# Kernel tuning notes

Hardware: AMD Instinct MI355X
Metric: run time of the kernel (lower is better)

Reference implementation:

```python
import jax, jax.numpy as jnp
import numpy as np

S, M, E, K, D = 16384, 512, 16, 2, 256
H1, H2, H3 = 500, 500, 1000


def setup_inputs() -> dict:
    key = jax.random.key(0)
    ks = jax.random.split(key, 8)
    p = lambda k, sh: jax.random.normal(k, sh, dtype=jnp.float32) * 0.02
    return {
        "x": jax.random.normal(ks[0], (S, M), dtype=jnp.float32),
        "noise": jax.random.uniform(ks[1], (S, E), dtype=jnp.float32),  # Router's torch.rand noise
        "Wr": p(ks[2], (E, M)),                       # router weight (Linear, no bias)
        "W1": p(ks[3], (E, M, H1)), "b1": jnp.zeros((E, H1), jnp.float32),
        "W2": p(ks[4], (E, H1, H2)), "b2": jnp.zeros((E, H2), jnp.float32),
        "W3": p(ks[5], (E, H2, H3)), "b3": jnp.zeros((E, H3), jnp.float32),
        "W4": p(ks[6], (E, H3, D)), "b4": jnp.zeros((E, D), jnp.float32),
    }


def reference(x, noise, Wr, W1, b1, W2, b2, W3, b3, W4, b4):
    # Router: zero-init linear + uniform noise
    logits = x @ Wr.T + noise                      # [S,E]
    select = jax.nn.softmax(logits, axis=1)        # [S,E]
    gate, index = jax.lax.top_k(select, K)         # [S,K]
    gate = gate / gate.sum(axis=1, keepdims=True)
    mask = jax.nn.one_hot(index, E, dtype=jnp.float32)  # [S,K,E]

    # load-balance loss
    density = mask.sum(axis=1).mean(axis=0)        # [E]
    density_proxy = select.mean(axis=0)            # [E]
    balance_loss = (density_proxy * density).mean() * float(E ** 2)

    # combine tensor: mask_flat is all-ones, so combine = sum_k gate_k * one_hot_k
    final_weight = (gate[:, :, None] * mask).sum(axis=1)     # [S,E]
    dispatch = (final_weight > 0).astype(x.dtype)            # bool->float, [S,E]
    select0 = dispatch

    # dense one-hot dispatch: expert_inputs[e,s,:] = x[s,:] * dispatch[s,e]
    expert_inputs = jnp.einsum('sm,se->esm', x, dispatch)    # [E,S,M]

    # per-expert Encoder MLP, vectorized over experts
    h = jax.nn.relu(jnp.einsum('esm,emh->esh', expert_inputs, W1) + b1[:, None, :])
    h = jax.nn.relu(jnp.einsum('esh,ehg->esg', h, W2) + b2[:, None, :])
    h = jax.nn.relu(jnp.einsum('esg,egf->esf', h, W3) + b3[:, None, :])
    expert_out = jnp.einsum('esf,efd->esd', h, W4) + b4[:, None, :]  # [E,S,D]

    final_output = jnp.einsum('se,esd->sd', final_weight, expert_out)  # [S,D]
    dist_loss = jnp.float32(0.0)  # t=False path
    return final_output, select0, balance_loss, dist_loss
```

## Files before the change

kernel.cpp:

```cpp
#include <hip/hip_runtime.h>
#include <stdint.h>

#define S_TOK 16384
#define M_DIM 512
#define E_EXP 16
#define D_OUT 256
#define H1D 500
#define H2D 500
#define H3D 1000

typedef float f32x4 __attribute__((ext_vector_type(4)));
typedef long lx2 __attribute__((ext_vector_type(2)));
typedef int i32x2 __attribute__((ext_vector_type(2)));

template <bool HI>
__device__ __forceinline__ int pk8(float a, float b, int old) {
  return __builtin_amdgcn_cvt_pk_fp8_f32(a, b, old, HI);
}
__device__ __forceinline__ unsigned char f2fp8(float f) {
  return (unsigned char)(__builtin_amdgcn_cvt_pk_fp8_f32(f, 0.f, 0, false) & 0xff);
}

__device__ __forceinline__ void ld_lds16(const unsigned char* g, unsigned char* l) {
  __builtin_amdgcn_global_load_lds(
      (const __attribute__((address_space(1))) unsigned int*)(const void*)g,
      (__attribute__((address_space(3))) unsigned int*)(void*)l, 16, 0, 0);
}

struct TokenRec { int i1, i2; float g1, g2; };

__global__ __launch_bounds__(256) void k_router(const float* __restrict__ x,
                                                const float* __restrict__ noise,
                                                const float* __restrict__ Wr,
                                                float* __restrict__ sel_out,
                                                float* __restrict__ sel_buf,
                                                TokenRec* __restrict__ te) {
  __shared__ float wr[E_EXP * 516];
  int t = threadIdx.x;
  for (int i = t; i < E_EXP * M_DIM; i += 256) {
    int e = i >> 9, m = i & 511;
    wr[e * 516 + m] = Wr[i];
  }
  __syncthreads();

  int wv = t >> 6, l = t & 63;
  int e = l & 15, tg = l >> 4;
  int s = blockIdx.x * 16 + wv * 4 + tg;

  const float* xr = x + (size_t)s * M_DIM;
  const float* wre = &wr[e * 516];
  double a0 = 0.0, a1 = 0.0, a2 = 0.0, a3 = 0.0;
#pragma unroll 4
  for (int m = 0; m < M_DIM; m += 4) {
    f32x4 xv = *(const f32x4*)(xr + m);
    f32x4 wv4 = *(const f32x4*)(wre + m);
    a0 += (double)xv.x * (double)wv4.x;
    a1 += (double)xv.y * (double)wv4.y;
    a2 += (double)xv.z * (double)wv4.z;
    a3 += (double)xv.w * (double)wv4.w;
  }
  double a = (a0 + a1) + (a2 + a3);
  a += (double)noise[(size_t)s * E_EXP + e];

  double mx = a;
#pragma unroll
  for (int off = 8; off >= 1; off >>= 1) { double o = __shfl_xor(mx, off, 64); mx = (o > mx) ? o : mx; }
  double p = exp(a - mx);
  double sum = p;
#pragma unroll
  for (int off = 8; off >= 1; off >>= 1) sum += __shfl_xor(sum, off, 64);
  sel_buf[(size_t)s * E_EXP + e] = (float)(p / sum);

  unsigned long long pb = __double_as_longlong(p);
  unsigned long long key = (pb & ~0xFFull) | (unsigned long long)(255 - e);
  unsigned long long k1 = key;
#pragma unroll
  for (int off = 8; off >= 1; off >>= 1) { unsigned long long o = __shfl_xor(k1, off, 64); k1 = (o > k1) ? o : k1; }
  int i1 = 255 - (int)(k1 & 0xFFull);
  unsigned long long key2 = (e == i1) ? 0ull : key;
  unsigned long long k2 = key2;
#pragma unroll
  for (int off = 8; off >= 1; off >>= 1) { unsigned long long o = __shfl_xor(k2, off, 64); k2 = (o > k2) ? o : k2; }
  int i2 = 255 - (int)(k2 & 0xFFull);

  double p1 = __shfl(p, tg * 16 + i1, 64);
  double p2 = __shfl(p, tg * 16 + i2, 64);

  sel_out[(size_t)s * E_EXP + e] = (e == i1 || e == i2) ? 1.f : 0.f;
  if (e == 0) {
    double inv = 1.0 / (p1 + p2);
    TokenRec r; r.i1 = i1; r.i2 = i2; r.g1 = (float)(p1 * inv); r.g2 = (float)(p2 * inv);
    te[s] = r;
  }
}

__global__ __launch_bounds__(256) void k_stats(const float* __restrict__ sel_buf,
                                               const TokenRec* __restrict__ te,
                                               float* __restrict__ partials) {
  __shared__ float psum[256];
  __shared__ unsigned int hist[E_EXP];
  int t = threadIdx.x, b = blockIdx.x;
  if (t < E_EXP) hist[t] = 0u;
  __syncthreads();
  int e = t & 15, rg = t >> 4;
  int base = b * 1024;
  float acc = 0.f;
#pragma unroll 4
  for (int i = 0; i < 64; i++)
    acc += sel_buf[(size_t)(base + i * 16 + rg) * E_EXP + e];
  for (int i = t; i < 1024; i += 256) {
    TokenRec r = te[base + i];
    atomicAdd(&hist[r.i1], 1u);
    atomicAdd(&hist[r.i2], 1u);
  }
  psum[t] = acc;
  __syncthreads();
  if (t < E_EXP) {
    float v = 0.f;
#pragma unroll
    for (int rg2 = 0; rg2 < 16; rg2++) v += psum[rg2 * 16 + t];
    partials[b * 32 + t] = v;
    partials[b * 32 + 16 + t] = (float)hist[t];
  }
}

__global__ void k_prefix_loss(const float* __restrict__ partials,
                              unsigned int* __restrict__ counts,
                              unsigned int* __restrict__ offsets,
                              unsigned int* __restrict__ cursor,
                              float* __restrict__ out_loss) {
  __shared__ float pr[E_EXP];
  __shared__ unsigned int cn[E_EXP];
  int t = threadIdx.x;
  if (t < E_EXP) {
    float p = 0.f, c = 0.f;
    for (int b = 0; b < 16; b++) { p += partials[b * 32 + t]; c += partials[b * 32 + 16 + t]; }
    pr[t] = p; cn[t] = (unsigned int)(c + 0.5f);
    cursor[t] = 0u;
  }
  __syncthreads();
  if (t == 0) {
    unsigned int acc = 0; float ls = 0.f;
    for (int e = 0; e < E_EXP; e++) {
      counts[e] = cn[e];
      offsets[e] = acc;
      acc += cn[e];
      ls += pr[e] * (float)cn[e];
    }
    out_loss[0] = ls * ((float)E_EXP / ((float)S_TOK * (float)S_TOK));
    out_loss[1] = 0.f;
  }
}

__global__ __launch_bounds__(256) void k_listbuild(const TokenRec* __restrict__ te,
                                                   const unsigned int* __restrict__ offsets,
                                                   unsigned int* __restrict__ cursor,
                                                   int* __restrict__ slot_token,
                                                   float* __restrict__ slot_gate,
                                                   int* __restrict__ tok_slot) {
  __shared__ unsigned int lhist[E_EXP];
  __shared__ unsigned int lbase[E_EXP];
  __shared__ unsigned int lcur[E_EXP];
  int t = threadIdx.x, b = blockIdx.x;
  int base = b * 1024;
  if (t < E_EXP) lhist[t] = 0u;
  __syncthreads();
  for (int i = t; i < 1024; i += 256) {
    TokenRec r = te[base + i];
    atomicAdd(&lhist[r.i1], 1u);
    atomicAdd(&lhist[r.i2], 1u);
  }
  __syncthreads();
  if (t < E_EXP) {
    lbase[t] = offsets[t] + atomicAdd(&cursor[t], lhist[t]);
    lcur[t] = 0u;
  }
  __syncthreads();
  for (int i = t; i < 1024; i += 256) {
    int s = base + i;
    TokenRec r = te[s];
    unsigned int p1 = atomicAdd(&lcur[r.i1], 1u);
    int sl1 = (int)(lbase[r.i1] + p1);
    slot_token[sl1] = s; slot_gate[sl1] = r.g1;
    unsigned int p2 = atomicAdd(&lcur[r.i2], 1u);
    int sl2 = (int)(lbase[r.i2] + p2);
    slot_token[sl2] = s; slot_gate[sl2] = r.g2;
    tok_slot[2 * s] = sl1;
    tok_slot[2 * s + 1] = sl2;
  }
}

__global__ __launch_bounds__(256) void k_gather(const float* __restrict__ x,
                                                const int* __restrict__ slot_token,
                                                unsigned char* __restrict__ xg) {
  int idx = blockIdx.x * 256 + threadIdx.x;
  int row = idx >> 6, t6 = idx & 63;
  int blk = t6 >> 3, q = (t6 >> 1) & 3, h = t6 & 1;
  int tkn = slot_token[row];
  const float* xp = x + (size_t)tkn * M_DIM + blk * 64 + h * 32 + q * 8;
  f32x4 v0 = *(const f32x4*)xp;
  f32x4 v1 = *(const f32x4*)(xp + 4);
  int b0 = pk8<false>(v0.x, v0.y, 0); b0 = pk8<true>(v0.z, v0.w, b0);
  int b1 = pk8<false>(v1.x, v1.y, 0); b1 = pk8<true>(v1.z, v1.w, b1);
  i32x2 o; o.x = b0; o.y = b1;
  *(i32x2*)&xg[(size_t)row * 512 + blk * 64 + q * 16 + h * 8] = o;
}

__global__ __launch_bounds__(256) void k_convw_all(const float* __restrict__ W1,
                                                   const float* __restrict__ W2,
                                                   const float* __restrict__ W3,
                                                   const float* __restrict__ W4,
                                                   unsigned char* __restrict__ D1,
                                                   unsigned char* __restrict__ D2,
                                                   unsigned char* __restrict__ D3,
                                                   unsigned char* __restrict__ D4) {
  __shared__ float tile[64][65];
  int tb = blockIdx.x, e = blockIdx.y;
  const float* src; unsigned char* dst;
  int Kr, Nr, Kp, Np, kx, ny;
  if (tb < 64)        { src = W1; dst = D1; Kr = 512;  Nr = H1D; Kp = 512;  Np = 512;  kx = tb >> 3;  ny = tb & 7; }
  else if (tb < 128)  { tb -= 64;  src = W2; dst = D2; Kr = H1D; Nr = H2D; Kp = 512;  Np = 512;  kx = tb >> 3;  ny = tb & 7; }
  else if (tb < 256)  { tb -= 128; src = W3; dst = D3; Kr = H2D; Nr = H3D; Kp = 512;  Np = 1024; kx = tb >> 4;  ny = tb & 15; }
  else                { tb -= 256; src = W4; dst = D4; Kr = H3D; Nr = 256; Kp = 1024; Np = 256;  kx = tb >> 2;  ny = tb & 3; }
  int k0 = kx * 64, n0 = ny * 64;
  int t = threadIdx.x;
  int cx = t & 63, ry = t >> 6;
  const float* sp = src + (size_t)e * Kr * Nr;
#pragma unroll
  for (int i = 0; i < 16; i++) {
    int k = k0 + ry + i * 4, n = n0 + cx;
    float v = (k < Kr && n < Nr) ? sp[(size_t)k * Nr + n] : 0.f;
    tile[ry + i * 4][cx] = v;
  }
  __syncthreads();
  int nl = t >> 2, q = t & 3;
  int b0 = pk8<false>(tile[q * 8 + 0][nl], tile[q * 8 + 1][nl], 0);
  b0 = pk8<true>(tile[q * 8 + 2][nl], tile[q * 8 + 3][nl], b0);
  int b1 = pk8<false>(tile[q * 8 + 4][nl], tile[q * 8 + 5][nl], 0);
  b1 = pk8<true>(tile[q * 8 + 6][nl], tile[q * 8 + 7][nl], b1);
  int c0 = pk8<false>(tile[32 + q * 8 + 0][nl], tile[32 + q * 8 + 1][nl], 0);
  c0 = pk8<true>(tile[32 + q * 8 + 2][nl], tile[32 + q * 8 + 3][nl], c0);
  int c1 = pk8<false>(tile[32 + q * 8 + 4][nl], tile[32 + q * 8 + 5][nl], 0);
  c1 = pk8<true>(tile[32 + q * 8 + 6][nl], tile[32 + q * 8 + 7][nl], c1);
  uint4 pk; pk.x = (unsigned)b0; pk.y = (unsigned)b1; pk.z = (unsigned)c0; pk.w = (unsigned)c1;
  *(uint4*)&dst[(size_t)e * Np * Kp + (size_t)(n0 + nl) * Kp + k0 + q * 16] = pk;
}

__global__ __launch_bounds__(256, 4) void k_gemm_mid(const unsigned char* __restrict__ in,
                                                  const unsigned char* __restrict__ wt,
                                                  const float* __restrict__ bias,
                                                  unsigned char* __restrict__ out,
                                                  const unsigned int* __restrict__ offsets,
                                                  const unsigned int* __restrict__ counts,
                                                  int KP, int NP, int NREAL) {
  int e = blockIdx.z;
  int n_e = (int)counts[e];
  if (n_e == 0) return;
  int base = (int)offsets[e];
  int bn = blockIdx.y;
  __shared__ __align__(16) unsigned char As[2][128 * 64];
  __shared__ __align__(16) unsigned char Bs[2][64 * 64];
  int t = threadIdx.x;
  int w = t >> 6, l = t & 63;
  int wm = w & 1, wn = w >> 1;
  int lr = l & 15, lq = l >> 4;
  int r_ = l >> 2, s_ = l & 3;
  int s2 = s_ ^ ((r_ >> 1) & 3);
  int rsw = (lq ^ ((lr >> 1) & 3)) * 16;
  int c0 = w * 2, c1 = w * 2 + 1;

  unsigned char* dA0[2] = {&As[0][c0 * 1024], &As[1][c0 * 1024]};
  unsigned char* dA1[2] = {&As[0][c1 * 1024], &As[1][c1 * 1024]};
  unsigned char* dB[2]  = {&Bs[0][w * 1024], &Bs[1][w * 1024]};

  const unsigned char* bW = wt + (size_t)e * NP * KP;
  const unsigned char* bsrc = bW + (size_t)(bn * 64 + w * 16 + r_) * KP + s2 * 16;
  int nk = KP >> 6;

  for (int bm = blockIdx.x; bm * 128 < n_e; bm += gridDim.x) {
    int ra = bm * 128 + c0 * 16 + r_; ra = (ra < n_e) ? ra : (n_e - 1);
    int rb = bm * 128 + c1 * 16 + r_; rb = (rb < n_e) ? rb : (n_e - 1);
    const unsigned char* a0 = in + (size_t)(base + ra) * KP + s2 * 16;
    const unsigned char* a1 = in + (size_t)(base + rb) * KP + s2 * 16;
    const unsigned char* bq = bsrc;
    f32x4 acc[4][2];
#pragma unroll
    for (int i = 0; i < 4; i++)
#pragma unroll
      for (int j = 0; j < 2; j++) acc[i][j] = (f32x4){0.f, 0.f, 0.f, 0.f};

    ld_lds16(a0, dA0[0]); ld_lds16(a1, dA1[0]); ld_lds16(bq, dB[0]);
    a0 += 64; a1 += 64; bq += 64;

    for (int ks = 0; ks < nk; ks++) {
      int cb = ks & 1, nb = cb ^ 1;
      __syncthreads();
      if (ks + 1 < nk) {
        ld_lds16(a0, dA0[nb]); ld_lds16(a1, dA1[nb]); ld_lds16(bq, dB[nb]);
        a0 += 64; a1 += 64; bq += 64;
      }
      lx2 af[4], bf[2];
#pragma unroll
      for (int mt = 0; mt < 4; mt++) af[mt] = *(const lx2*)&As[cb][(wm * 64 + mt * 16 + lr) * 64 + rsw];
#pragma unroll
      for (int nt = 0; nt < 2; nt++) bf[nt] = *(const lx2*)&Bs[cb][(wn * 32 + nt * 16 + lr) * 64 + rsw];
#pragma unroll
      for (int mt = 0; mt < 4; mt++)
#pragma unroll
        for (int nt = 0; nt < 2; nt++) {
          acc[mt][nt] = __builtin_amdgcn_mfma_f32_16x16x32_fp8_fp8(af[mt].x, bf[nt].x, acc[mt][nt], 0, 0, 0);
          acc[mt][nt] = __builtin_amdgcn_mfma_f32_16x16x32_fp8_fp8(af[mt].y, bf[nt].y, acc[mt][nt], 0, 0, 0);
        }
    }

#pragma unroll
    for (int nt = 0; nt < 2; nt++) {
      int col = bn * 64 + wn * 32 + nt * 16 + lr;
      bool cok = col < NREAL;
      float bv = cok ? bias[(size_t)e * NREAL + col] : 0.f;
      int kl = col & 63;
      int pb = ((kl >> 3) & 3) * 16 + ((kl >> 5) & 1) * 8 + (kl & 7);
#pragma unroll
      for (int mt = 0; mt < 4; mt++)
#pragma unroll
        for (int reg = 0; reg < 4; reg++) {
          int r = bm * 128 + wm * 64 + mt * 16 + lq * 4 + reg;
          if (r < n_e) {
            float v = cok ? fmaxf(acc[mt][nt][reg] + bv, 0.f) : 0.f;
            out[(size_t)(base + r) * NP + bn * 64 + pb] = f2fp8(v);
          }
        }
    }
  }
}

__global__ __launch_bounds__(256, 4) void k_gemm_fin(const unsigned char* __restrict__ in,
                                                  const unsigned char* __restrict__ wt,
                                                  const float* __restrict__ bias,
                                                  float* __restrict__ eo,
                                                  const unsigned int* __restrict__ offsets,
                                                  const unsigned int* __restrict__ counts,
                                                  const float* __restrict__ slot_gate) {
  const int KP = 1024, NP = 256;
  int e = blockIdx.z;
  int n_e = (int)counts[e];
  if (n_e == 0) return;
  int base = (int)offsets[e];
  int bn = blockIdx.y;
  __shared__ __align__(16) unsigned char As[2][64 * 64];
  __shared__ __align__(16) unsigned char Bs[2][64 * 64];
  int t = threadIdx.x;
  int w = t >> 6, l = t & 63;
  int wm = w & 1, wn = w >> 1;
  int lr = l & 15, lq = l >> 4;
  int r_ = l >> 2, s_ = l & 3;
  int s2 = s_ ^ ((r_ >> 1) & 3);
  int rsw = (lq ^ ((lr >> 1) & 3)) * 16;

  unsigned char* dA[2] = {&As[0][w * 1024], &As[1][w * 1024]};
  unsigned char* dB[2] = {&Bs[0][w * 1024], &Bs[1][w * 1024]};

  const unsigned char* bW = wt + (size_t)e * NP * KP;
  const unsigned char* bsrc = bW + (size_t)(bn * 64 + w * 16 + r_) * KP + s2 * 16;
  int nk = KP >> 6;

  for (int bm = blockIdx.x; bm * 64 < n_e; bm += gridDim.x) {
    int ra = bm * 64 + w * 16 + r_; ra = (ra < n_e) ? ra : (n_e - 1);
    const unsigned char* a0 = in + (size_t)(base + ra) * KP + s2 * 16;
    const unsigned char* bq = bsrc;
    f32x4 acc[2][2];
#pragma unroll
    for (int i = 0; i < 2; i++)
#pragma unroll
      for (int j = 0; j < 2; j++) acc[i][j] = (f32x4){0.f, 0.f, 0.f, 0.f};

    ld_lds16(a0, dA[0]); ld_lds16(bq, dB[0]);
    a0 += 64; bq += 64;

    for (int ks = 0; ks < nk; ks++) {
      int cb = ks & 1, nb = cb ^ 1;
      __syncthreads();
      if (ks + 1 < nk) {
        ld_lds16(a0, dA[nb]); ld_lds16(bq, dB[nb]);
        a0 += 64; bq += 64;
      }
      lx2 af[2], bf[2];
#pragma unroll
      for (int mt = 0; mt < 2; mt++) af[mt] = *(const lx2*)&As[cb][(wm * 32 + mt * 16 + lr) * 64 + rsw];
#pragma unroll
      for (int nt = 0; nt < 2; nt++) bf[nt] = *(const lx2*)&Bs[cb][(wn * 32 + nt * 16 + lr) * 64 + rsw];
#pragma unroll
      for (int mt = 0; mt < 2; mt++)
#pragma unroll
        for (int nt = 0; nt < 2; nt++) {
          acc[mt][nt] = __builtin_amdgcn_mfma_f32_16x16x32_fp8_fp8(af[mt].x, bf[nt].x, acc[mt][nt], 0, 0, 0);
          acc[mt][nt] = __builtin_amdgcn_mfma_f32_16x16x32_fp8_fp8(af[mt].y, bf[nt].y, acc[mt][nt], 0, 0, 0);
        }
    }

#pragma unroll
    for (int mt = 0; mt < 2; mt++)
#pragma unroll
      for (int reg = 0; reg < 4; reg++) {
        int r = bm * 64 + wm * 32 + mt * 16 + lq * 4 + reg;
        if (r < n_e) {
          int gr = base + r;
          float g = slot_gate[gr];
#pragma unroll
          for (int nt = 0; nt < 2; nt++) {
            int col = bn * 64 + wn * 32 + nt * 16 + lr;
            eo[(size_t)gr * NP + col] = g * (acc[mt][nt][reg] + bias[(size_t)e * 256 + col]);
          }
        }
      }
  }
}

__global__ __launch_bounds__(256) void k_combine(const float* __restrict__ eo,
                                                 const int* __restrict__ tok_slot,
                                                 float* __restrict__ out) {
  int idx = blockIdx.x * 256 + threadIdx.x;
  int s = idx >> 6, q = idx & 63;
  int sl1 = tok_slot[2 * s], sl2 = tok_slot[2 * s + 1];
  f32x4 v1 = *(const f32x4*)&eo[(size_t)sl1 * D_OUT + q * 4];
  f32x4 v2 = *(const f32x4*)&eo[(size_t)sl2 * D_OUT + q * 4];
  *(f32x4*)&out[(size_t)s * D_OUT + q * 4] = v1 + v2;
}

extern "C" void kernel_launch(void* const* d_in, const int* in_sizes, int n_in,
                              void* d_out, int out_size, void* d_ws, size_t ws_size,
                              hipStream_t stream) {
  const float* x    = (const float*)d_in[0];
  const float* nois = (const float*)d_in[1];
  const float* Wr   = (const float*)d_in[2];
  const float* W1   = (const float*)d_in[3];
  const float* b1   = (const float*)d_in[4];
  const float* W2   = (const float*)d_in[5];
  const float* b2   = (const float*)d_in[6];
  const float* W3   = (const float*)d_in[7];
  const float* b3   = (const float*)d_in[8];
  const float* W4   = (const float*)d_in[9];
  const float* b4   = (const float*)d_in[10];
  float* out = (float*)d_out;

  char* w = (char*)d_ws;
  unsigned char* actA = (unsigned char*)(w + 0);
  unsigned char* actB = (unsigned char*)(w + 33554432);
  unsigned char* Wt1  = (unsigned char*)(w + 50331648);
  unsigned char* Wt2  = (unsigned char*)(w + 54525952);
  unsigned char* Wt3  = (unsigned char*)(w + 58720256);
  unsigned char* Wt4  = (unsigned char*)(w + 67108864);
  float*         eo   = (float*)(w + 71303168);
  int*           slot_token = (int*)(w + 104857600);
  float*         slot_gate  = (float*)(w + 104988672);
  TokenRec*      te         = (TokenRec*)(w + 105119744);
  unsigned int*  counts  = (unsigned int*)(w + 105381888);
  unsigned int*  cursor  = (unsigned int*)(w + 105381952);
  unsigned int*  offsets = (unsigned int*)(w + 105382016);
  int*           tok_slot = (int*)(w + 105382080);
  float*         sel_buf  = (float*)(w + 0);
  float*         partials = (float*)(w + 1048576);

  float* sel_out  = out + (size_t)S_TOK * D_OUT;
  float* loss_out = out + (size_t)S_TOK * D_OUT + (size_t)S_TOK * E_EXP;

  k_convw_all<<<dim3(320, E_EXP), dim3(256), 0, stream>>>(W1, W2, W3, W4, Wt1, Wt2, Wt3, Wt4);

  k_router<<<dim3(S_TOK / 16), dim3(256), 0, stream>>>(x, nois, Wr, sel_out, sel_buf, te);
  k_stats<<<dim3(16), dim3(256), 0, stream>>>(sel_buf, te, partials);
  k_prefix_loss<<<dim3(1), dim3(64), 0, stream>>>(partials, counts, offsets, cursor, loss_out);
  k_listbuild<<<dim3(16), dim3(256), 0, stream>>>(te, offsets, cursor, slot_token, slot_gate, tok_slot);
  k_gather<<<dim3((2 * S_TOK * 64) / 256), dim3(256), 0, stream>>>(x, slot_token, actB);

  k_gemm_mid<<<dim3(24, 8, E_EXP), dim3(256), 0, stream>>>(actB, Wt1, b1, actA, offsets, counts, 512, 512, H1D);
  k_gemm_mid<<<dim3(24, 8, E_EXP), dim3(256), 0, stream>>>(actA, Wt2, b2, actB, offsets, counts, 512, 512, H2D);
  k_gemm_mid<<<dim3(24, 16, E_EXP), dim3(256), 0, stream>>>(actB, Wt3, b3, actA, offsets, counts, 512, 1024, H3D);
  k_gemm_fin<<<dim3(32, 4, E_EXP), dim3(256), 0, stream>>>(actA, Wt4, b4, eo, offsets, counts, slot_gate);
  k_combine<<<dim3(S_TOK * 64 / 256), dim3(256), 0, stream>>>(eo, tok_slot, out);

  (void)in_sizes; (void)n_in; (void)out_size; (void)ws_size;
}
```

Baseline: 379.0 us.

## Keep expert weight tile resident in registers across M-tiles in mid GEMMs

The mid-layer FP8 GEMM now loads each block's full 64xK weight slice into registers once, instead of streaming it through double-buffered LDS on every K step. The block then loops over several 128-row token tiles while reusing that slice. The grid's M dimension is cut from 24 to 8 so each block covers more row tiles and amortizes the weight load, and launch bounds drop to 3 waves per SIMD to make room for the extra registers. K is hardcoded to 512 and the K loop is fully unrolled. The trade-off is higher register pressure, lower occupancy and fewer blocks, which could hurt latency hiding.

```diff
diff --git a/kernel.cpp b/kernel.cpp
--- a/kernel.cpp
+++ b/kernel.cpp
@@ -246,20 +246,20 @@
   *(uint4*)&dst[(size_t)e * Np * Kp + (size_t)(n0 + nl) * Kp + k0 + q * 16] = pk;
 }
 
-__global__ __launch_bounds__(256, 4) void k_gemm_mid(const unsigned char* __restrict__ in,
+__global__ __launch_bounds__(256, 3) void k_gemm_mid(const unsigned char* __restrict__ in,
                                                   const unsigned char* __restrict__ wt,
                                                   const float* __restrict__ bias,
                                                   unsigned char* __restrict__ out,
                                                   const unsigned int* __restrict__ offsets,
                                                   const unsigned int* __restrict__ counts,
-                                                  int KP, int NP, int NREAL) {
+                                                  int NP, int NREAL) {
+  const int KP = 512, NK = 8;
   int e = blockIdx.z;
   int n_e = (int)counts[e];
   if (n_e == 0) return;
   int base = (int)offsets[e];
   int bn = blockIdx.y;
   __shared__ __align__(16) unsigned char As[2][128 * 64];
-  __shared__ __align__(16) unsigned char Bs[2][64 * 64];
   int t = threadIdx.x;
   int w = t >> 6, l = t & 63;
   int wm = w & 1, wn = w >> 1;
@@ -271,45 +271,48 @@
 
   unsigned char* dA0[2] = {&As[0][c0 * 1024], &As[1][c0 * 1024]};
   unsigned char* dA1[2] = {&As[0][c1 * 1024], &As[1][c1 * 1024]};
-  unsigned char* dB[2]  = {&Bs[0][w * 1024], &Bs[1][w * 1024]};
 
   const unsigned char* bW = wt + (size_t)e * NP * KP;
-  const unsigned char* bsrc = bW + (size_t)(bn * 64 + w * 16 + r_) * KP + s2 * 16;
-  int nk = KP >> 6;
+  lx2 barr[2][NK];
+#pragma unroll
+  for (int nt = 0; nt < 2; nt++) {
+    const unsigned char* brow = bW + (size_t)(bn * 64 + wn * 32 + nt * 16 + lr) * KP + lq * 16;
+#pragma unroll
+    for (int ks = 0; ks < NK; ks++)
+      barr[nt][ks] = *(const lx2*)(brow + ks * 64);
+  }
 
   for (int bm = blockIdx.x; bm * 128 < n_e; bm += gridDim.x) {
     int ra = bm * 128 + c0 * 16 + r_; ra = (ra < n_e) ? ra : (n_e - 1);
     int rb = bm * 128 + c1 * 16 + r_; rb = (rb < n_e) ? rb : (n_e - 1);
     const unsigned char* a0 = in + (size_t)(base + ra) * KP + s2 * 16;
     const unsigned char* a1 = in + (size_t)(base + rb) * KP + s2 * 16;
-    const unsigned char* bq = bsrc;
     f32x4 acc[4][2];
 #pragma unroll
     for (int i = 0; i < 4; i++)
 #pragma unroll
       for (int j = 0; j < 2; j++) acc[i][j] = (f32x4){0.f, 0.f, 0.f, 0.f};
 
-    ld_lds16(a0, dA0[0]); ld_lds16(a1, dA1[0]); ld_lds16(bq, dB[0]);
-    a0 += 64; a1 += 64; bq += 64;
-
-    for (int ks = 0; ks < nk; ks++) {
+    ld_lds16(a0, dA0[0]); ld_lds16(a1, dA1[0]);
+    a0 += 64; a1 += 64;
+
+#pragma unroll
+    for (int ks = 0; ks < NK; ks++) {
       int cb = ks & 1, nb = cb ^ 1;
       __syncthreads();
-      if (ks + 1 < nk) {
-        ld_lds16(a0, dA0[nb]); ld_lds16(a1, dA1[nb]); ld_lds16(bq, dB[nb]);
-        a0 += 64; a1 += 64; bq += 64;
+      if (ks + 1 < NK) {
+        ld_lds16(a0, dA0[nb]); ld_lds16(a1, dA1[nb]);
+        a0 += 64; a1 += 64;
       }
-      lx2 af[4], bf[2];
+      lx2 af[4];
 #pragma unroll
       for (int mt = 0; mt < 4; mt++) af[mt] = *(const lx2*)&As[cb][(wm * 64 + mt * 16 + lr) * 64 + rsw];
 #pragma unroll
-      for (int nt = 0; nt < 2; nt++) bf[nt] = *(const lx2*)&Bs[cb][(wn * 32 + nt * 16 + lr) * 64 + rsw];
-#pragma unroll
       for (int mt = 0; mt < 4; mt++)
 #pragma unroll
         for (int nt = 0; nt < 2; nt++) {
-          acc[mt][nt] = __builtin_amdgcn_mfma_f32_16x16x32_fp8_fp8(af[mt].x, bf[nt].x, acc[mt][nt], 0, 0, 0);
-          acc[mt][nt] = __builtin_amdgcn_mfma_f32_16x16x32_fp8_fp8(af[mt].y, bf[nt].y, acc[mt][nt], 0, 0, 0);
+          acc[mt][nt] = __builtin_amdgcn_mfma_f32_16x16x32_fp8_fp8(af[mt].x, barr[nt][ks].x, acc[mt][nt], 0, 0, 0);
+          acc[mt][nt] = __builtin_amdgcn_mfma_f32_16x16x32_fp8_fp8(af[mt].y, barr[nt][ks].y, acc[mt][nt], 0, 0, 0);
         }
     }
 
@@ -472,9 +475,9 @@
   k_listbuild<<<dim3(16), dim3(256), 0, stream>>>(te, offsets, cursor, slot_token, slot_gate, tok_slot);
   k_gather<<<dim3((2 * S_TOK * 64) / 256), dim3(256), 0, stream>>>(x, slot_token, actB);
 
-  k_gemm_mid<<<dim3(24, 8, E_EXP), dim3(256), 0, stream>>>(actB, Wt1, b1, actA, offsets, counts, 512, 512, H1D);
-  k_gemm_mid<<<dim3(24, 8, E_EXP), dim3(256), 0, stream>>>(actA, Wt2, b2, actB, offsets, counts, 512, 512, H2D);
-  k_gemm_mid<<<dim3(24, 16, E_EXP), dim3(256), 0, stream>>>(actB, Wt3, b3, actA, offsets, counts, 512, 1024, H3D);
+  k_gemm_mid<<<dim3(8, 8, E_EXP), dim3(256), 0, stream>>>(actB, Wt1, b1, actA, offsets, counts, 512, H1D);
+  k_gemm_mid<<<dim3(8, 8, E_EXP), dim3(256), 0, stream>>>(actA, Wt2, b2, actB, offsets, counts, 512, H2D);
+  k_gemm_mid<<<dim3(8, 16, E_EXP), dim3(256), 0, stream>>>(actB, Wt3, b3, actA, offsets, counts, 1024, H3D);
   k_gemm_fin<<<dim3(32, 4, E_EXP), dim3(256), 0, stream>>>(actA, Wt4, b4, eo, offsets, counts, slot_gate);
   k_combine<<<dim3(S_TOK * 64 / 256), dim3(256), 0, stream>>>(eo, tok_slot, out);
 
```

Measured after the change: 428.0 us. 12.9% more time.
